# Optimization experiments

Measured on AMD Instinct MI355X. Metric: run time of the kernel, lower is better.

## Reference

```python
import jax, jax.numpy as jnp
import numpy as np

N = 50000
E = 800000
IN_DIM = 128
F_NUM = 64
OUT_DIM = 16


def gcn_norm(edge_index, edge_weight, num_nodes):
    # add self loops with fill value 1.0 (improved=False), then symmetric norm
    e = edge_index.shape[1]
    w = jnp.ones((e,), jnp.float32) if edge_weight is None else edge_weight
    loop = jnp.arange(num_nodes, dtype=edge_index.dtype)
    row = jnp.concatenate([edge_index[0], loop])
    col = jnp.concatenate([edge_index[1], loop])
    w = jnp.concatenate([w, jnp.ones((num_nodes,), jnp.float32)])
    deg = jax.ops.segment_sum(w, col, num_segments=num_nodes)
    dis = jnp.where(deg > 0, jax.lax.rsqrt(jnp.where(deg > 0, deg, 1.0)), 0.0)
    norm = dis[row] * w * dis[col]
    return row, col, norm


def dgconv(x, edge_index, edge_weight, num_nodes):
    row, col, norm = gcn_norm(edge_index, edge_weight, num_nodes)
    # gather -> scale -> scatter-add
    msg = norm[:, None] * x[row]          # [E+N, F]
    return jax.ops.segment_sum(msg, col, num_segments=num_nodes)


def setup_inputs() -> dict:
    key = jax.random.key(0)
    ks = jax.random.split(key, 12)
    x = jax.random.normal(ks[0], (N, IN_DIM), jnp.float32)
    edge_index = jax.random.randint(ks[1], (2, E), 0, N, jnp.int64 if jax.config.jax_enable_x64 else jnp.int32)
    edge_in = jax.random.randint(ks[2], (2, E), 0, N, edge_index.dtype)
    edge_out = jax.random.randint(ks[3], (2, E), 0, N, edge_index.dtype)
    in_w = jax.random.uniform(ks[4], (E,), jnp.float32)
    out_w = jax.random.uniform(ks[5], (E,), jnp.float32)
    lin1_w = jax.random.normal(ks[6], (F_NUM, IN_DIM), jnp.float32) / np.sqrt(IN_DIM)
    lin2_w = jax.random.normal(ks[7], (F_NUM, 3 * F_NUM), jnp.float32) / np.sqrt(3 * F_NUM)
    bias1 = jnp.zeros((1, F_NUM), jnp.float32)
    bias2 = jnp.zeros((1, F_NUM), jnp.float32)
    conv_w = jax.random.normal(ks[8], (OUT_DIM, 3 * F_NUM), jnp.float32) / np.sqrt(3 * F_NUM)
    conv_b = jnp.zeros((OUT_DIM,), jnp.float32)
    return {"x": x, "edge_index": edge_index, "edge_in": edge_in, "edge_out": edge_out,
            "in_w": in_w, "out_w": out_w, "lin1_w": lin1_w, "lin2_w": lin2_w,
            "bias1": bias1, "bias2": bias2, "conv_w": conv_w, "conv_b": conv_b}


def reference(x, edge_index, edge_in, edge_out, in_w, out_w,
              lin1_w, lin2_w, bias1, bias2, conv_w, conv_b):
    n = x.shape[0]
    h = x @ lin1_w.T                                          # [N, F]
    h1 = dgconv(h, edge_index, None, n) + bias1
    h2 = dgconv(h, edge_in, in_w, n) + bias1
    h3 = dgconv(h, edge_out, out_w, n) + bias1
    h = jax.nn.relu(jnp.concatenate([h1, h2, h3], axis=-1))   # [N, 3F]
    h = h @ lin2_w.T                                          # [N, F]
    h1 = dgconv(h, edge_index, None, n) + bias2
    h2 = dgconv(h, edge_in, in_w, n) + bias2
    h3 = dgconv(h, edge_out, out_w, n) + bias2
    h = jax.nn.relu(jnp.concatenate([h1, h2, h3], axis=-1))   # [N, 3F]
    # Conv1d(kernel_size=1) == pointwise linear over channels
    logits = h @ conv_w.T + conv_b                            # [N, out_dim]
    return jax.nn.log_softmax(logits, axis=1)
```

## Files before the change

### kernel.cpp

```cpp
#include <hip/hip_runtime.h>
#include <hip/hip_fp16.h>
#include <math.h>

#define FDIM 64
#define CATDIM 192
#define CH 2048
#define MAXNB 1024
#define SCTILE 2048


__global__ __launch_bounds__(256) void k_chist(const int* __restrict__ ei0,
                                               const int* __restrict__ ei1,
                                               const int* __restrict__ ei2,
                                               int* __restrict__ bhT,
                                               int NB, int nchunks, int E) {
    __shared__ int hist[MAXNB];
    const int c = blockIdx.x, g = blockIdx.y, tid = threadIdx.x;
    const int* dest = (g == 0 ? ei0 : g == 1 ? ei1 : ei2) + E;
    const size_t L = (size_t)NB * nchunks;

    for (int i = tid; i < NB; i += 256) hist[i] = 0;
    __syncthreads();

    const int lo = c * CH, hi = min(E, lo + CH);
    for (int i = lo + tid; i < hi; i += 256) atomicAdd(&hist[dest[i] >> 6], 1);
    __syncthreads();

    for (int i = tid; i < NB; i += 256)
        bhT[g * L + (size_t)c * NB + i] = hist[i];
}


__global__ __launch_bounds__(256) void k_tr(const int* __restrict__ in,
                                            int* __restrict__ out,
                                            int rows, int cols) {
    __shared__ int tile[32][33];
    const int g = blockIdx.z;
    const int c0 = blockIdx.x * 32;
    const int r0 = blockIdx.y * 32;
    const int tx = threadIdx.x & 31, ty0 = threadIdx.x >> 5;
    const size_t L = (size_t)rows * cols;
    const int* pin = in + (size_t)g * L;
    int* pout = out + (size_t)g * L;

    for (int dy = 0; dy < 32; dy += 8) {
        int r = r0 + ty0 + dy, c = c0 + tx;
        tile[ty0 + dy][tx] = (r < rows && c < cols) ? pin[(size_t)r * cols + c] : 0;
    }
    __syncthreads();
    for (int dy = 0; dy < 32; dy += 8) {
        int c = c0 + ty0 + dy, r = r0 + tx;
        if (c < cols && r < rows) pout[(size_t)c * rows + r] = tile[tx][ty0 + dy];
    }
}


__global__ __launch_bounds__(256) void k_scan_a(const int* __restrict__ bh,
                                                int* __restrict__ bsum,
                                                int L, int nblkS) {
    __shared__ int s[256];
    const int b = blockIdx.x, g = blockIdx.y, tid = threadIdx.x;
    const int* data = bh + (size_t)g * L;
    const int base = b * SCTILE + tid * 8;
    int v = 0;
#pragma unroll
    for (int j = 0; j < 8; ++j) {
        int idx = base + j;
        if (idx < L) v += data[idx];
    }
    s[tid] = v;
    __syncthreads();
    for (int d = 128; d > 0; d >>= 1) {
        if (tid < d) s[tid] += s[tid + d];
        __syncthreads();
    }
    if (tid == 0) bsum[g * nblkS + b] = s[0];
}

__global__ __launch_bounds__(256) void k_scan_b(int* __restrict__ bsum, int nblkS) {
    __shared__ int s[256];
    const int g = blockIdx.x, tid = threadIdx.x;
    int v = (tid < nblkS) ? bsum[g * nblkS + tid] : 0;
    s[tid] = v;
    __syncthreads();
    for (int d = 1; d < 256; d <<= 1) {
        int t = (tid >= d) ? s[tid - d] : 0;
        __syncthreads();
        s[tid] += t;
        __syncthreads();
    }
    if (tid < nblkS) bsum[g * nblkS + tid] = s[tid] - v;
}

__global__ __launch_bounds__(256) void k_scan_c(int* __restrict__ bh,
                                                const int* __restrict__ bsum,
                                                int L, int nblkS) {
    __shared__ int s[256];
    const int b = blockIdx.x, g = blockIdx.y, tid = threadIdx.x;
    int* data = bh + (size_t)g * L;
    const int base = b * SCTILE + tid * 8;

    int e[8];
    int tot = 0;
#pragma unroll
    for (int j = 0; j < 8; ++j) {
        e[j] = (base + j < L) ? data[base + j] : 0;
        tot += e[j];
    }
    s[tid] = tot;
    __syncthreads();
    for (int d = 1; d < 256; d <<= 1) {
        int t = (tid >= d) ? s[tid - d] : 0;
        __syncthreads();
        s[tid] += t;
        __syncthreads();
    }
    int run = bsum[g * nblkS + b] + s[tid] - tot;
#pragma unroll
    for (int j = 0; j < 8; ++j) {
        if (base + j < L) {
            int v = e[j];
            data[base + j] = run;
            run += v;
        }
    }
}


__global__ void k_bbase(const int* __restrict__ bh, int* __restrict__ bbase,
                        int NB, int nchunks, int E) {
    int i = blockIdx.x * blockDim.x + threadIdx.x;
    if (i >= 3 * NB) return;
    int g = i / NB, b = i - g * NB;
    bbase[g * (NB + 1) + b] = bh[((size_t)g * NB + b) * nchunks];
    if (b == 0) bbase[g * (NB + 1) + NB] = E;
}


__global__ __launch_bounds__(256) void k_cfill(const int* __restrict__ ei0,
                                               const int* __restrict__ ei1,
                                               const int* __restrict__ ei2,
                                               const float* __restrict__ w1,
                                               const float* __restrict__ w2,
                                               const int* __restrict__ bhT2,
                                               int2* __restrict__ barr,
                                               int NB, int nchunks, int E) {
    __shared__ int cur[MAXNB];
    const int c = blockIdx.x, g = blockIdx.y, tid = threadIdx.x;
    const int* e = (g == 0 ? ei0 : g == 1 ? ei1 : ei2);
    const float* w = (g == 1 ? w1 : w2);
    const int* srcp = e;
    const int* dest = e + E;
    int2* bout = barr + (size_t)g * E;
    const size_t L = (size_t)NB * nchunks;

    for (int i = tid; i < NB; i += 256)
        cur[i] = bhT2[g * L + (size_t)c * NB + i];
    __syncthreads();

    const int lo = c * CH, hi = min(E, lo + CH);
    for (int i = lo + tid; i < hi; i += 256) {
        int d = dest[i];
        int slot = atomicAdd(&cur[d >> 6], 1);
        float wv = (g == 0) ? 0.f : w[i];
        bout[slot] = make_int2(srcp[i] | ((d & 63) << 16), __float_as_int(wv));
    }
}


__global__ __launch_bounds__(256) void k_deg(const int2* __restrict__ barr,
                                             const int* __restrict__ bbase,
                                             int* __restrict__ rowptr,
                                             float* __restrict__ dis,
                                             int N, int E, int NB) {
    __shared__ int hist[64];
    __shared__ float wsum[64];
    __shared__ int sc[64];

    const int b = blockIdx.x, g = blockIdx.y, tid = threadIdx.x;
    const int2* bin = barr + (size_t)g * E;
    const int beg = bbase[g * (NB + 1) + b];
    const int end = bbase[g * (NB + 1) + b + 1];

    if (tid < 64) { hist[tid] = 0; wsum[tid] = 1.0f; }
    __syncthreads();

    for (int t = beg + tid; t < end; t += 256) {
        int2 p = bin[t];
        int dl = (p.x >> 16) & 63;
        atomicAdd(&hist[dl], 1);
        if (g) atomicAdd(&wsum[dl], __int_as_float(p.y));
    }
    __syncthreads();

    if (tid < 64) sc[tid] = hist[tid];
    __syncthreads();
    for (int d = 1; d < 64; d <<= 1) {
        int t = 0;
        if (tid < 64 && tid >= d) t = sc[tid - d];
        __syncthreads();
        if (tid < 64) sc[tid] += t;
        __syncthreads();
    }
    if (tid < 64) {
        int node = b * 64 + tid;
        if (node < N) {
            rowptr[g * (N + 1) + node] = beg + (sc[tid] - hist[tid]);
            float s = g ? wsum[tid] : (1.0f + (float)hist[tid]);
            dis[g * N + node] = rsqrtf(s);
        }
    }
    if (b == NB - 1 && tid == 0) rowptr[g * (N + 1) + N] = end;
}


__global__ __launch_bounds__(256) void k_place(const int2* __restrict__ barr,
                                               const int* __restrict__ bbase,
                                               const int* __restrict__ rowptr,
                                               const float* __restrict__ dis,
                                               unsigned* __restrict__ csr,
                                               int N, int E, int NB) {
    __shared__ int cur[64];
    const int b = blockIdx.x, g = blockIdx.y, tid = threadIdx.x;
    const int2* bin = barr + (size_t)g * E;
    const int beg = bbase[g * (NB + 1) + b];
    const int end = bbase[g * (NB + 1) + b + 1];

    if (tid < 64) {
        int node = b * 64 + tid;
        cur[tid] = (node < N) ? rowptr[g * (N + 1) + node] - beg : 0;
    }
    __syncthreads();

    for (int t = beg + tid; t < end; t += 256) {
        int2 p = bin[t];
        int dl = (p.x >> 16) & 63;
        int pos = atomicAdd(&cur[dl], 1);
        int src = p.x & 0xFFFF;
        float wv = g ? __int_as_float(p.y) : 1.0f;
        float v = wv * dis[g * N + src];
        unsigned short wb = __half_as_ushort(__float2half(v));
        csr[(size_t)g * E + beg + pos] = (unsigned)src | ((unsigned)wb << 16);
    }
}


template <typename T> __device__ inline float4 load4f(const T* p);
template <> __device__ inline float4 load4f<float>(const float* p) {
    return *reinterpret_cast<const float4*>(p);
}
template <> __device__ inline float4 load4f<__half>(const __half* p) {
    __half2 a = *reinterpret_cast<const __half2*>(p);
    __half2 b = *reinterpret_cast<const __half2*>(p + 2);
    float2 fa = __half22float2(a), fb = __half22float2(b);
    return make_float4(fa.x, fa.y, fb.x, fb.y);
}

template <int K, typename TA>
__global__ __launch_bounds__(256) void k_gemm(const TA* __restrict__ A,
                                              const float* __restrict__ W,
                                              __half* __restrict__ out, int n) {
    __shared__ float wt[K * 65];
    __shared__ float xs[64 * 36];

    const int tid = threadIdx.x;
    const int n0 = blockIdx.x * 64;

    for (int idx = tid; idx < FDIM * K; idx += 256) {
        int fr = idx / K;
        int kr = idx - fr * K;
        wt[kr * 65 + fr] = W[idx];
    }

    const int f = tid & 63;
    const int q = tid >> 6;
    float acc[16];
#pragma unroll
    for (int j = 0; j < 16; ++j) acc[j] = 0.f;

    for (int kc = 0; kc < K; kc += 32) {
        __syncthreads();
#pragma unroll
        for (int u = tid; u < 512; u += 256) {
            int node = u >> 3;
            int k4 = u & 7;
            int gn = n0 + node;
            float4 a = make_float4(0.f, 0.f, 0.f, 0.f);
            if (gn < n) a = load4f(&A[(size_t)gn * K + kc + k4 * 4]);
            *reinterpret_cast<float4*>(&xs[node * 36 + k4 * 4]) = a;
        }
        __syncthreads();

#pragma unroll
        for (int kk = 0; kk < 32; kk += 4) {
            float w0 = wt[(kc + kk + 0) * 65 + f];
            float w1 = wt[(kc + kk + 1) * 65 + f];
            float w2 = wt[(kc + kk + 2) * 65 + f];
            float w3 = wt[(kc + kk + 3) * 65 + f];
#pragma unroll
            for (int jj = 0; jj < 16; ++jj) {
                int j = jj * 4 + q;
                float4 av = *reinterpret_cast<const float4*>(&xs[j * 36 + kk]);
                acc[jj] = fmaf(av.x, w0, fmaf(av.y, w1, fmaf(av.z, w2, fmaf(av.w, w3, acc[jj]))));
            }
        }
    }

#pragma unroll
    for (int jj = 0; jj < 16; ++jj) {
        int node = n0 + jj * 4 + q;
        if (node < n) out[(size_t)node * FDIM + f] = __float2half(acc[jj]);
    }
}


__global__ __launch_bounds__(256) void k_gather(const __half* __restrict__ h,
                                                const float* __restrict__ dis,
                                                const int* __restrict__ rowptr,
                                                const unsigned* __restrict__ csr,
                                                const float* __restrict__ bias,
                                                __half* __restrict__ cat,
                                                int N, int E) {
    int i = blockIdx.x * 4 + (threadIdx.x >> 6);
    if (i >= N) return;
    const int lane = threadIdx.x & 63;

    const float hv = __half2float(h[(size_t)i * FDIM + lane]);
    const float b = bias[lane];

#pragma unroll
    for (int g = 0; g < 3; ++g) {
        const int* rp = rowptr + g * (N + 1);
        const unsigned* cg = csr + (size_t)g * E;
        const int beg = __builtin_amdgcn_readfirstlane(rp[i]);
        const int end = __builtin_amdgcn_readfirstlane(rp[i + 1]);
        float dg = dis[g * N + i];

        float acc0 = 0.f, acc1 = 0.f, acc2 = 0.f, acc3 = 0.f;
        float acc4 = 0.f, acc5 = 0.f, acc6 = 0.f, acc7 = 0.f;
        int j = beg;
        for (; j + 8 <= end; j += 8) {
            unsigned u0 = cg[j + 0];
            unsigned u1 = cg[j + 1];
            unsigned u2 = cg[j + 2];
            unsigned u3 = cg[j + 3];
            unsigned u4 = cg[j + 4];
            unsigned u5 = cg[j + 5];
            unsigned u6 = cg[j + 6];
            unsigned u7 = cg[j + 7];
            float a0 = __half2float(h[(size_t)(u0 & 0xFFFFu) * FDIM + lane]);
            float a1 = __half2float(h[(size_t)(u1 & 0xFFFFu) * FDIM + lane]);
            float a2 = __half2float(h[(size_t)(u2 & 0xFFFFu) * FDIM + lane]);
            float a3 = __half2float(h[(size_t)(u3 & 0xFFFFu) * FDIM + lane]);
            float a4 = __half2float(h[(size_t)(u4 & 0xFFFFu) * FDIM + lane]);
            float a5 = __half2float(h[(size_t)(u5 & 0xFFFFu) * FDIM + lane]);
            float a6 = __half2float(h[(size_t)(u6 & 0xFFFFu) * FDIM + lane]);
            float a7 = __half2float(h[(size_t)(u7 & 0xFFFFu) * FDIM + lane]);
            acc0 = fmaf(__half2float(__ushort_as_half((unsigned short)(u0 >> 16))), a0, acc0);
            acc1 = fmaf(__half2float(__ushort_as_half((unsigned short)(u1 >> 16))), a1, acc1);
            acc2 = fmaf(__half2float(__ushort_as_half((unsigned short)(u2 >> 16))), a2, acc2);
            acc3 = fmaf(__half2float(__ushort_as_half((unsigned short)(u3 >> 16))), a3, acc3);
            acc4 = fmaf(__half2float(__ushort_as_half((unsigned short)(u4 >> 16))), a4, acc4);
            acc5 = fmaf(__half2float(__ushort_as_half((unsigned short)(u5 >> 16))), a5, acc5);
            acc6 = fmaf(__half2float(__ushort_as_half((unsigned short)(u6 >> 16))), a6, acc6);
            acc7 = fmaf(__half2float(__ushort_as_half((unsigned short)(u7 >> 16))), a7, acc7);
        }
        if (j + 4 <= end) {
            unsigned u0 = cg[j + 0];
            unsigned u1 = cg[j + 1];
            unsigned u2 = cg[j + 2];
            unsigned u3 = cg[j + 3];
            float a0 = __half2float(h[(size_t)(u0 & 0xFFFFu) * FDIM + lane]);
            float a1 = __half2float(h[(size_t)(u1 & 0xFFFFu) * FDIM + lane]);
            float a2 = __half2float(h[(size_t)(u2 & 0xFFFFu) * FDIM + lane]);
            float a3 = __half2float(h[(size_t)(u3 & 0xFFFFu) * FDIM + lane]);
            acc0 = fmaf(__half2float(__ushort_as_half((unsigned short)(u0 >> 16))), a0, acc0);
            acc1 = fmaf(__half2float(__ushort_as_half((unsigned short)(u1 >> 16))), a1, acc1);
            acc2 = fmaf(__half2float(__ushort_as_half((unsigned short)(u2 >> 16))), a2, acc2);
            acc3 = fmaf(__half2float(__ushort_as_half((unsigned short)(u3 >> 16))), a3, acc3);
            j += 4;
        }
        for (; j < end; ++j) {
            unsigned u0 = cg[j];
            float a0 = __half2float(h[(size_t)(u0 & 0xFFFFu) * FDIM + lane]);
            acc0 = fmaf(__half2float(__ushort_as_half((unsigned short)(u0 >> 16))), a0, acc0);
        }
        float outv = dg * (((acc0 + acc1) + (acc2 + acc3)) + ((acc4 + acc5) + (acc6 + acc7)))
                   + dg * dg * hv + b;
        cat[(size_t)i * CATDIM + g * FDIM + lane] = __float2half(outv > 0.f ? outv : 0.f);
    }
}


__global__ __launch_bounds__(256) void k_final(const __half* __restrict__ cat,
                                               const float* __restrict__ convw,
                                               const float* __restrict__ convb,
                                               float* __restrict__ out, int n) {
    __shared__ float wl[16 * 196];
    __shared__ float bl[16];
    const int tid = threadIdx.x;
    for (int t = tid; t < 16 * 192; t += 256) {
        int o = t / 192;
        int k = t - o * 192;
        wl[o * 196 + k] = convw[t];
    }
    if (tid < 16) bl[tid] = convb[tid];
    __syncthreads();

    const int o = tid & 15;
    const int node = blockIdx.x * 16 + (tid >> 4);
    const int nc = node < n ? node : n - 1;

    const float4* xr4 = reinterpret_cast<const float4*>(cat + (size_t)nc * CATDIM);
    const float* wr = &wl[o * 196];
    float acc = bl[o];
#pragma unroll
    for (int k8 = 0; k8 < CATDIM / 8; ++k8) {
        float4 raw = xr4[k8];
        const __half2* hp = reinterpret_cast<const __half2*>(&raw);
        float2 f0 = __half22float2(hp[0]);
        float2 f1 = __half22float2(hp[1]);
        float2 f2 = __half22float2(hp[2]);
        float2 f3 = __half22float2(hp[3]);
        const float* w8 = wr + k8 * 8;
        acc += f0.x * w8[0] + f0.y * w8[1] + f1.x * w8[2] + f1.y * w8[3] +
               f2.x * w8[4] + f2.y * w8[5] + f3.x * w8[6] + f3.y * w8[7];
    }

    float m = acc;
    m = fmaxf(m, __shfl_xor(m, 1));
    m = fmaxf(m, __shfl_xor(m, 2));
    m = fmaxf(m, __shfl_xor(m, 4));
    m = fmaxf(m, __shfl_xor(m, 8));
    float s = __expf(acc - m);
    s += __shfl_xor(s, 1);
    s += __shfl_xor(s, 2);
    s += __shfl_xor(s, 4);
    s += __shfl_xor(s, 8);
    if (node < n) out[(size_t)node * 16 + o] = acc - m - logf(s);
}


extern "C" void kernel_launch(void* const* d_in, const int* in_sizes, int n_in,
                              void* d_out, int out_size, void* d_ws, size_t ws_size,
                              hipStream_t stream) {
    const float* x      = (const float*)d_in[0];
    const int*   ei     = (const int*)d_in[1];
    const int*   e_in   = (const int*)d_in[2];
    const int*   e_out  = (const int*)d_in[3];
    const float* in_w   = (const float*)d_in[4];
    const float* out_w  = (const float*)d_in[5];
    const float* lin1_w = (const float*)d_in[6];
    const float* lin2_w = (const float*)d_in[7];
    const float* bias1  = (const float*)d_in[8];
    const float* bias2  = (const float*)d_in[9];
    const float* conv_w = (const float*)d_in[10];
    const float* conv_b = (const float*)d_in[11];
    float* out = (float*)d_out;

    const int N = in_sizes[0] / 128;
    const int E = in_sizes[1] / 2;
    const int NB = (N + 63) >> 6;
    const int nchunks = (E + CH - 1) / CH;
    const int L = NB * nchunks;
    const int nblkS = (L + SCTILE - 1) / SCTILE;

    float* ws = (float*)d_ws;
    size_t o = 0;
    float* dis    = ws + o;            o += (size_t)3 * N;
    int*   rowptr = (int*)(ws + o);    o += ((size_t)3 * (N + 1) + 1) & ~1ull;
    int*   bbase  = (int*)(ws + o);    o += ((size_t)3 * (NB + 1) + 1) & ~1ull;
    int*   bsum   = (int*)(ws + o);    o += ((size_t)3 * nblkS + 1) & ~1ull;
    int*   bh     = (int*)(ws + o);    o += ((size_t)3 * L + 3) & ~3ull;
    int*   bhT    = (int*)(ws + o);    o += ((size_t)3 * L + 3) & ~3ull;
    __half* h     = (__half*)(ws + o); o += (size_t)N * (FDIM / 2);
    o = (o + 3) & ~3ull;
    unsigned* csr = (unsigned*)(ws + o); o += (size_t)3 * E;
    o = (o + 3) & ~3ull;
    __half* cat   = (__half*)(ws + o); o += (size_t)N * (CATDIM / 2);
    int2*  barr   = (int2*)cat;

    const int B = 256;

    hipLaunchKernelGGL(k_chist, dim3(nchunks, 3), dim3(B), 0, stream, ei, e_in, e_out, bhT, NB, nchunks, E);
    hipLaunchKernelGGL(k_tr, dim3((NB + 31) / 32, (nchunks + 31) / 32, 3), dim3(B), 0, stream,
                       bhT, bh, nchunks, NB);
    hipLaunchKernelGGL(k_scan_a, dim3(nblkS, 3), dim3(B), 0, stream, bh, bsum, L, nblkS);
    hipLaunchKernelGGL(k_scan_b, dim3(3), dim3(B), 0, stream, bsum, nblkS);
    hipLaunchKernelGGL(k_scan_c, dim3(nblkS, 3), dim3(B), 0, stream, bh, bsum, L, nblkS);
    hipLaunchKernelGGL(k_bbase, dim3((3 * NB + B - 1) / B), dim3(B), 0, stream, bh, bbase, NB, nchunks, E);
    hipLaunchKernelGGL(k_tr, dim3((nchunks + 31) / 32, (NB + 31) / 32, 3), dim3(B), 0, stream,
                       bh, bhT, NB, nchunks);
    hipLaunchKernelGGL(k_cfill, dim3(nchunks, 3), dim3(B), 0, stream,
                       ei, e_in, e_out, in_w, out_w, bhT, barr, NB, nchunks, E);
    hipLaunchKernelGGL(k_deg, dim3(NB, 3), dim3(B), 0, stream, barr, bbase, rowptr, dis, N, E, NB);
    hipLaunchKernelGGL(k_place, dim3(NB, 3), dim3(B), 0, stream, barr, bbase, rowptr, dis, csr, N, E, NB);

    hipLaunchKernelGGL((k_gemm<128, float>), dim3((N + 63) / 64), dim3(B), 0, stream, x, lin1_w, h, N);
    hipLaunchKernelGGL(k_gather, dim3((N + 3) / 4), dim3(B), 0, stream,
                       h, dis, rowptr, csr, bias1, cat, N, E);

    hipLaunchKernelGGL((k_gemm<192, __half>), dim3((N + 63) / 64), dim3(B), 0, stream, cat, lin2_w, h, N);
    hipLaunchKernelGGL(k_gather, dim3((N + 3) / 4), dim3(B), 0, stream,
                       h, dis, rowptr, csr, bias2, cat, N, E);

    hipLaunchKernelGGL(k_final, dim3((N + 15) / 16), dim3(B), 0, stream, cat, conv_w, conv_b, out, N);
}
```

Measured before the change: 413.7 us.

## Drop histogram transposes, fold bucket bases into scan, chunk GEMM weights in LDS

The chunk histogram kernel now writes bucket-major counts directly, and the fill kernel reads them strided. That removes both transpose kernels. The bucket-base extraction moves into the final scan kernel, which drops another launch. The GEMM loads its weight tile in K-chunks (64 or 96 rows) instead of the whole matrix. This cuts LDS use, which may allow more resident blocks, at the cost of extra reloads and strided histogram writes and reads.

```diff
diff --git a/kernel.cpp b/kernel.cpp
--- a/kernel.cpp
+++ b/kernel.cpp
@@ -12,12 +12,11 @@
 __global__ __launch_bounds__(256) void k_chist(const int* __restrict__ ei0,
                                                const int* __restrict__ ei1,
                                                const int* __restrict__ ei2,
-                                               int* __restrict__ bhT,
+                                               int* __restrict__ bh,
                                                int NB, int nchunks, int E) {
     __shared__ int hist[MAXNB];
     const int c = blockIdx.x, g = blockIdx.y, tid = threadIdx.x;
     const int* dest = (g == 0 ? ei0 : g == 1 ? ei1 : ei2) + E;
-    const size_t L = (size_t)NB * nchunks;
 
     for (int i = tid; i < NB; i += 256) hist[i] = 0;
     __syncthreads();
@@ -27,31 +26,7 @@
     __syncthreads();
 
     for (int i = tid; i < NB; i += 256)
-        bhT[g * L + (size_t)c * NB + i] = hist[i];
-}
-
-
-__global__ __launch_bounds__(256) void k_tr(const int* __restrict__ in,
-                                            int* __restrict__ out,
-                                            int rows, int cols) {
-    __shared__ int tile[32][33];
-    const int g = blockIdx.z;
-    const int c0 = blockIdx.x * 32;
-    const int r0 = blockIdx.y * 32;
-    const int tx = threadIdx.x & 31, ty0 = threadIdx.x >> 5;
-    const size_t L = (size_t)rows * cols;
-    const int* pin = in + (size_t)g * L;
-    int* pout = out + (size_t)g * L;
-
-    for (int dy = 0; dy < 32; dy += 8) {
-        int r = r0 + ty0 + dy, c = c0 + tx;
-        tile[ty0 + dy][tx] = (r < rows && c < cols) ? pin[(size_t)r * cols + c] : 0;
-    }
-    __syncthreads();
-    for (int dy = 0; dy < 32; dy += 8) {
-        int c = c0 + ty0 + dy, r = r0 + tx;
-        if (c < cols && r < rows) pout[(size_t)c * rows + r] = tile[tx][ty0 + dy];
-    }
+        bh[((size_t)g * NB + i) * nchunks + c] = hist[i];
 }
 
 
@@ -92,9 +67,12 @@
     if (tid < nblkS) bsum[g * nblkS + tid] = s[tid] - v;
 }
 
+
 __global__ __launch_bounds__(256) void k_scan_c(int* __restrict__ bh,
                                                 const int* __restrict__ bsum,
-                                                int L, int nblkS) {
+                                                int* __restrict__ bbase,
+                                                int L, int nblkS,
+                                                int NB, int nchunks, int E) {
     __shared__ int s[256];
     const int b = blockIdx.x, g = blockIdx.y, tid = threadIdx.x;
     int* data = bh + (size_t)g * L;
@@ -118,22 +96,15 @@
     int run = bsum[g * nblkS + b] + s[tid] - tot;
 #pragma unroll
     for (int j = 0; j < 8; ++j) {
-        if (base + j < L) {
+        int idx = base + j;
+        if (idx < L) {
             int v = e[j];
-            data[base + j] = run;
+            data[idx] = run;
+            if (idx % nchunks == 0) bbase[g * (NB + 1) + idx / nchunks] = run;
             run += v;
         }
     }
-}
-
-
-__global__ void k_bbase(const int* __restrict__ bh, int* __restrict__ bbase,
-                        int NB, int nchunks, int E) {
-    int i = blockIdx.x * blockDim.x + threadIdx.x;
-    if (i >= 3 * NB) return;
-    int g = i / NB, b = i - g * NB;
-    bbase[g * (NB + 1) + b] = bh[((size_t)g * NB + b) * nchunks];
-    if (b == 0) bbase[g * (NB + 1) + NB] = E;
+    if (b == 0 && tid == 0) bbase[g * (NB + 1) + NB] = E;
 }
 
 
@@ -142,7 +113,7 @@
                                                const int* __restrict__ ei2,
                                                const float* __restrict__ w1,
                                                const float* __restrict__ w2,
-                                               const int* __restrict__ bhT2,
+                                               const int* __restrict__ bhs,
                                                int2* __restrict__ barr,
                                                int NB, int nchunks, int E) {
     __shared__ int cur[MAXNB];
@@ -152,10 +123,9 @@
     const int* srcp = e;
     const int* dest = e + E;
     int2* bout = barr + (size_t)g * E;
-    const size_t L = (size_t)NB * nchunks;
 
     for (int i = tid; i < NB; i += 256)
-        cur[i] = bhT2[g * L + (size_t)c * NB + i];
+        cur[i] = bhs[((size_t)g * NB + i) * nchunks + c];
     __syncthreads();
 
     const int lo = c * CH, hi = min(E, lo + CH);
@@ -256,21 +226,15 @@
     return make_float4(fa.x, fa.y, fb.x, fb.y);
 }
 
-template <int K, typename TA>
+template <int K, int KCH, typename TA>
 __global__ __launch_bounds__(256) void k_gemm(const TA* __restrict__ A,
                                               const float* __restrict__ W,
                                               __half* __restrict__ out, int n) {
-    __shared__ float wt[K * 65];
+    __shared__ float wt[KCH * 65];
     __shared__ float xs[64 * 36];
 
     const int tid = threadIdx.x;
     const int n0 = blockIdx.x * 64;
-
-    for (int idx = tid; idx < FDIM * K; idx += 256) {
-        int fr = idx / K;
-        int kr = idx - fr * K;
-        wt[kr * 65 + fr] = W[idx];
-    }
 
     const int f = tid & 63;
     const int q = tid >> 6;
@@ -280,6 +244,13 @@
 
     for (int kc = 0; kc < K; kc += 32) {
         __syncthreads();
+        if ((kc % KCH) == 0) {
+            for (int idx = tid; idx < FDIM * KCH; idx += 256) {
+                int fr = idx / KCH;
+                int kr = idx - fr * KCH;
+                wt[kr * 65 + fr] = W[fr * K + kc + kr];
+            }
+        }
 #pragma unroll
         for (int u = tid; u < 512; u += 256) {
             int node = u >> 3;
@@ -291,12 +262,13 @@
         }
         __syncthreads();
 
+        const int kb = kc % KCH;
 #pragma unroll
         for (int kk = 0; kk < 32; kk += 4) {
-            float w0 = wt[(kc + kk + 0) * 65 + f];
-            float w1 = wt[(kc + kk + 1) * 65 + f];
-            float w2 = wt[(kc + kk + 2) * 65 + f];
-            float w3 = wt[(kc + kk + 3) * 65 + f];
+            float w0 = wt[(kb + kk + 0) * 65 + f];
+            float w1 = wt[(kb + kk + 1) * 65 + f];
+            float w2 = wt[(kb + kk + 2) * 65 + f];
+            float w3 = wt[(kb + kk + 3) * 65 + f];
 #pragma unroll
             for (int jj = 0; jj < 16; ++jj) {
                 int j = jj * 4 + q;
@@ -472,7 +444,6 @@
     int*   bbase  = (int*)(ws + o);    o += ((size_t)3 * (NB + 1) + 1) & ~1ull;
     int*   bsum   = (int*)(ws + o);    o += ((size_t)3 * nblkS + 1) & ~1ull;
     int*   bh     = (int*)(ws + o);    o += ((size_t)3 * L + 3) & ~3ull;
-    int*   bhT    = (int*)(ws + o);    o += ((size_t)3 * L + 3) & ~3ull;
     __half* h     = (__half*)(ws + o); o += (size_t)N * (FDIM / 2);
     o = (o + 3) & ~3ull;
     unsigned* csr = (unsigned*)(ws + o); o += (size_t)3 * E;
@@ -482,25 +453,20 @@
 
     const int B = 256;
 
-    hipLaunchKernelGGL(k_chist, dim3(nchunks, 3), dim3(B), 0, stream, ei, e_in, e_out, bhT, NB, nchunks, E);
-    hipLaunchKernelGGL(k_tr, dim3((NB + 31) / 32, (nchunks + 31) / 32, 3), dim3(B), 0, stream,
-                       bhT, bh, nchunks, NB);
+    hipLaunchKernelGGL(k_chist, dim3(nchunks, 3), dim3(B), 0, stream, ei, e_in, e_out, bh, NB, nchunks, E);
     hipLaunchKernelGGL(k_scan_a, dim3(nblkS, 3), dim3(B), 0, stream, bh, bsum, L, nblkS);
     hipLaunchKernelGGL(k_scan_b, dim3(3), dim3(B), 0, stream, bsum, nblkS);
-    hipLaunchKernelGGL(k_scan_c, dim3(nblkS, 3), dim3(B), 0, stream, bh, bsum, L, nblkS);
-    hipLaunchKernelGGL(k_bbase, dim3((3 * NB + B - 1) / B), dim3(B), 0, stream, bh, bbase, NB, nchunks, E);
-    hipLaunchKernelGGL(k_tr, dim3((nchunks + 31) / 32, (NB + 31) / 32, 3), dim3(B), 0, stream,
-                       bh, bhT, NB, nchunks);
+    hipLaunchKernelGGL(k_scan_c, dim3(nblkS, 3), dim3(B), 0, stream, bh, bsum, bbase, L, nblkS, NB, nchunks, E);
     hipLaunchKernelGGL(k_cfill, dim3(nchunks, 3), dim3(B), 0, stream,
-                       ei, e_in, e_out, in_w, out_w, bhT, barr, NB, nchunks, E);
+                       ei, e_in, e_out, in_w, out_w, bh, barr, NB, nchunks, E);
     hipLaunchKernelGGL(k_deg, dim3(NB, 3), dim3(B), 0, stream, barr, bbase, rowptr, dis, N, E, NB);
     hipLaunchKernelGGL(k_place, dim3(NB, 3), dim3(B), 0, stream, barr, bbase, rowptr, dis, csr, N, E, NB);
 
-    hipLaunchKernelGGL((k_gemm<128, float>), dim3((N + 63) / 64), dim3(B), 0, stream, x, lin1_w, h, N);
+    hipLaunchKernelGGL((k_gemm<128, 64, float>), dim3((N + 63) / 64), dim3(B), 0, stream, x, lin1_w, h, N);
     hipLaunchKernelGGL(k_gather, dim3((N + 3) / 4), dim3(B), 0, stream,
                        h, dis, rowptr, csr, bias1, cat, N, E);
 
-    hipLaunchKernelGGL((k_gemm<192, __half>), dim3((N + 63) / 64), dim3(B), 0, stream, cat, lin2_w, h, N);
+    hipLaunchKernelGGL((k_gemm<192, 96, __half>), dim3((N + 63) / 64), dim3(B), 0, stream, cat, lin2_w, h, N);
     hipLaunchKernelGGL(k_gather, dim3((N + 3) / 4), dim3(B), 0, stream,
                        h, dis, rowptr, csr, bias2, cat, N, E);
 
```

After: 393.3 us. -4.9%, faster.
